# Optimization experiments

Hardware: AMD Instinct MI355X
Metric: run time of the kernel (lower is better)

## Reference

```python
import jax, jax.numpy as jnp
import numpy as np

H = 512        # hidden_dim
D_IN = 512     # input_dim
N_ACT = 16     # output_dim
DICT = 8192    # dict_len (episodic memory slots)
B = 4096       # batch
N_CYCLES = 10  # LCA iterations
DT_T = 0.6     # LCA dt/tau
EPS = 1e-8     # cosine-similarity eps


def setup_inputs() -> dict:
    key = jax.random.key(0)
    ks = jax.random.split(key, 12)
    NHT = 4 * H + 3  # (N_VSIG+1)*H + N_SSIG
    s = lambda i, shape, sc=1.0: jax.random.normal(ks[i], shape, jnp.float32) * sc
    return {
        "x_t": s(0, (1, B, D_IN)),
        "h_prev": s(1, (1, B, H), 0.1),
        "c_prev": s(2, (1, B, H), 0.1),
        "W_i2h": s(3, (NHT, D_IN), 1.0 / np.sqrt(D_IN)),
        "b_i2h": jnp.zeros((NHT,), jnp.float32),
        "W_h2h": s(4, (NHT, H), 1.0 / np.sqrt(H)),
        "b_h2h": jnp.zeros((NHT,), jnp.float32),
        "vals": s(5, (DICT, H), 0.1),  # episodic memory table
        "W_ih": s(6, (H, H), 1.0 / np.sqrt(H)),
        "b_ih": jnp.zeros((H,), jnp.float32),
        "W_actor": s(7, (N_ACT, H), 1.0 / np.sqrt(H)),
        "b_actor": jnp.zeros((N_ACT,), jnp.float32),
        "W_critic": s(8, (1, H), 1.0 / np.sqrt(H)),
        "b_critic": jnp.zeros((1,), jnp.float32),
        "mem_ptr": 0,
    }


def _lca(sim, leak, comp, w_input):
    # Leaky competing accumulator over memory slots; sim:[B,DICT], scalars:[B,1]
    ff = w_input * sim
    def step(V, _):
        inhib = comp * (jnp.sum(V, axis=-1, keepdims=True) - V)  # lateral inhibition (excl. self)
        V = jax.nn.relu(V + DT_T * (ff - leak * V - inhib))
        return V, None
    V, _ = jax.lax.scan(step, jnp.zeros_like(sim), None, length=N_CYCLES)
    return V


def reference(x_t, h_prev, c_prev, W_i2h, b_i2h, W_h2h, b_h2h, vals,
              W_ih, b_ih, W_actor, b_actor, W_critic, b_critic, mem_ptr):
    x, h, c = x_t[0], h_prev[0], c_prev[0]  # [B, dim]
    preact = x @ W_i2h.T + b_i2h + h @ W_h2h.T + b_h2h  # [B, 4H+3]
    gates = jax.nn.sigmoid(preact[:, :3 * H])
    f_t = gates[:, :H]
    o_t = gates[:, H:2 * H]
    i_t = gates[:, 2 * H:3 * H]
    inps = jax.nn.sigmoid(preact[:, 3 * H + 0])[:, None]  # input strength (gain=1)
    leak = jax.nn.sigmoid(preact[:, 3 * H + 1])[:, None]
    comp = jax.nn.sigmoid(preact[:, 3 * H + 2])[:, None]
    c_new = jnp.tanh(preact[:, 3 * H + 3:])
    c_t = c * f_t + i_t * c_new
    # --- recall: cosine similarity vs memory, then LCA competition ---
    qn = jnp.linalg.norm(c_t, axis=-1, keepdims=True)        # [B,1]
    mn = jnp.linalg.norm(vals, axis=-1, keepdims=True)       # [DICT,1]
    sim = (c_t @ vals.T) / jnp.maximum(qn * mn.T, EPS)       # [B,DICT]
    w = _lca(sim, leak, comp, inps)                          # [B,DICT]
    m_t = w @ vals                                           # [B,H]
    cm_t = c_t + m_t
    # --- encode: ring-buffer scatter write of cm_t into memory ---
    idx = (mem_ptr + jnp.arange(B)) % DICT
    new_vals = vals.at[idx].set(cm_t)
    h_t = o_t * jnp.tanh(cm_t)
    # --- A2C head ---
    a2c_h = jax.nn.relu(h_t @ W_ih.T + b_ih)
    pi = jax.nn.softmax(a2c_h @ W_actor.T + b_actor, axis=-1)
    value = a2c_h @ W_critic.T + b_critic
    return pi, value, h_t, cm_t, m_t, new_vals
```

## Files before the change

### kernel.cpp

```cpp
#include <hip/hip_runtime.h>
#include <hip/hip_fp16.h>
#include <math.h>

#define HH    512
#define DICT  8192
#define BATCH 4096
#define NCYC  10
#define DTT   0.6f

#define BM  128
#define BKT 64

using f16x8 = __attribute__((ext_vector_type(8))) _Float16;
using f32x4 = __attribute__((ext_vector_type(4))) float;

__device__ __forceinline__ float sigmoidf_(float x) { return 1.0f / (1.0f + __expf(-x)); }

__device__ __forceinline__ float waveReduceSum(float v) {
#pragma unroll
  for (int o = 1; o < 64; o <<= 1) v += __shfl_xor(v, o);
  return v;
}

__device__ __forceinline__ void gld16(const void* g, void* l) {
  __builtin_amdgcn_global_load_lds(
      (const __attribute__((address_space(1))) void*)g,
      (__attribute__((address_space(3))) void*)l, 16, 0, 0);
}

template<int N> __device__ __forceinline__ void vmwait() {
  if constexpr (N == 8)      asm volatile("s_waitcnt vmcnt(8)" ::: "memory");
  else if constexpr (N == 6) asm volatile("s_waitcnt vmcnt(6)" ::: "memory");
  else if constexpr (N == 4) asm volatile("s_waitcnt vmcnt(4)" ::: "memory");
  else if constexpr (N == 3) asm volatile("s_waitcnt vmcnt(3)" ::: "memory");
  else                       asm volatile("s_waitcnt vmcnt(0)" ::: "memory");
  __builtin_amdgcn_sched_barrier(0);
}

__device__ __forceinline__ void blockbar() {
  asm volatile("" ::: "memory");
  __builtin_amdgcn_s_barrier();
  __builtin_amdgcn_sched_barrier(0);
}

template<int ROWS>
__device__ __forceinline__ void stage_tile(const __half* gbase, int ld, char* lds, int tid) {
  constexpr int ISS = ROWS * 8 / 256;
#pragma unroll
  for (int i = 0; i < ISS; ++i) {
    int cidx = i * 256 + tid;
    int row  = cidx >> 3;
    int slot = cidx & 7;
    int k4   = slot ^ (row & 7);
    gld16(gbase + (size_t)row * ld + k4 * 8, lds + cidx * 16);
  }
}

__device__ __forceinline__ f16x8 frag_ld(const char* lds, int row, int kchunk) {
  int slot = kchunk ^ (row & 7);
  return *(const f16x8*)(lds + row * 128 + slot * 16);
}

template<int FN>
__device__ __forceinline__ void tile_mfma(const char* As, const char* Bs,
                                          int lane, int wr, int wc, f32x4 (&acc)[4][FN]) {
  const int g = lane >> 4, r = lane & 15;
#pragma unroll
  for (int ks = 0; ks < 2; ++ks) {
    f16x8 af[4], bfr[FN];
#pragma unroll
    for (int i = 0; i < 4; ++i)
      af[i] = frag_ld(As, wr * 64 + i * 16 + r, ks * 4 + g);
#pragma unroll
    for (int j = 0; j < FN; ++j)
      bfr[j] = frag_ld(Bs, wc * (FN * 16) + j * 16 + r, ks * 4 + g);
#pragma unroll
    for (int i = 0; i < 4; ++i)
#pragma unroll
      for (int j = 0; j < FN; ++j)
        acc[i][j] = __builtin_amdgcn_mfma_f32_16x16x32_f16(af[i], bfr[j], acc[i][j], 0, 0, 0);
  }
}

template<int BN, int FN>
__device__ __forceinline__ void gemm_seg(const __half* A, int lda, const __half* B, int ldb,
                                         int m0, int n0, int K, char* lds, int tid,
                                         f32x4 (&acc)[4][FN]) {
  constexpr int ABYTES = BM * BKT * 2;
  constexpr int BBYTES = BN * BKT * 2;
  constexpr int BUF = ABYTES + BBYTES;
  constexpr int NL = (BM + BN) * 8 / 256;
  const int lane = tid & 63, wid = tid >> 6;
  const int wr = wid >> 1, wc = wid & 1;
  const int nt = K / BKT;
  const __half* Ab = A + (size_t)m0 * lda;
  const __half* Bb = B + (size_t)n0 * ldb;
  stage_tile<BM>(Ab, lda, lds, tid);
  stage_tile<BN>(Bb, ldb, lds + ABYTES, tid);
  int cur = 0;
  for (int t = 0; t < nt; ++t) {
    char* curb = lds + cur * BUF;
    if (t + 1 < nt) {
      char* nxt = lds + (cur ^ 1) * BUF;
      stage_tile<BM>(Ab + (t + 1) * BKT, lda, nxt, tid);
      stage_tile<BN>(Bb + (t + 1) * BKT, ldb, nxt + ABYTES, tid);
      vmwait<NL>();
    } else {
      vmwait<0>();
    }
    blockbar();
    tile_mfma<FN>(curb, curb + ABYTES, lane, wr, wc, acc);
    blockbar();
    cur ^= 1;
  }
}

__device__ __forceinline__ void zero_acc4(f32x4 (&a)[4][4]) {
  f32x4 z = {0.f, 0.f, 0.f, 0.f};
#pragma unroll
  for (int i = 0; i < 4; ++i)
#pragma unroll
    for (int j = 0; j < 4; ++j) a[i][j] = z;
}
__device__ __forceinline__ void zero_acc2(f32x4 (&a)[4][2]) {
  f32x4 z = {0.f, 0.f, 0.f, 0.f};
#pragma unroll
  for (int i = 0; i < 4; ++i)
#pragma unroll
    for (int j = 0; j < 2; ++j) a[i][j] = z;
}

template<int ROWS, int NT>
__device__ __forceinline__ void stage32(const __half* gbase, int ld, char* lds, int tid) {
  constexpr int HALF = ROWS / 2;
  constexpr int ISS = ROWS * 4 / NT;
#pragma unroll
  for (int i = 0; i < ISS; ++i) {
    int cidx = i * NT + tid;
    int line = cidx >> 3;
    int slot = cidx & 7;
    int t    = slot ^ (line & 7);
    int row  = line + HALF * (t >> 2);
    int k4   = t & 3;
    gld16(gbase + (size_t)row * ld + k4 * 8, lds + cidx * 16);
  }
}

template<int HALF>
__device__ __forceinline__ f16x8 frag32(const char* lds, int row, int g) {
  int line = row & (HALF - 1);
  int t    = g + 4 * (row / HALF);
  int slot = t ^ (line & 7);
  return *(const f16x8*)(lds + line * 128 + slot * 16);
}

template<int MF, int NF, int AHALF, int BHALF>
__device__ __forceinline__ void tile_mfma32(const char* As, const char* Bs,
                                            int arow0, int brow0, int lane,
                                            f32x4 (&acc)[MF][NF]) {
  const int g = lane >> 4, r = lane & 15;
  f16x8 af[MF], bf[NF];
#pragma unroll
  for (int i = 0; i < MF; ++i) af[i] = frag32<AHALF>(As, arow0 + i * 16 + r, g);
#pragma unroll
  for (int j = 0; j < NF; ++j) bf[j] = frag32<BHALF>(Bs, brow0 + j * 16 + r, g);
#pragma unroll
  for (int i = 0; i < MF; ++i)
#pragma unroll
    for (int j = 0; j < NF; ++j)
      acc[i][j] = __builtin_amdgcn_mfma_f32_16x16x32_f16(af[i], bf[j], acc[i][j], 0, 0, 0);
}

__global__ __launch_bounds__(256) void k_prep(
    const float* __restrict__ x, const float* __restrict__ h,
    const float* __restrict__ Wi, const float* __restrict__ Wh, const float* __restrict__ Wih,
    const float* __restrict__ vals, const int* __restrict__ mptr,
    __half* __restrict__ x_h, __half* __restrict__ h_h,
    __half* __restrict__ Wip_h, __half* __restrict__ Whp_h, __half* __restrict__ Wih_h,
    float* __restrict__ nv, __half* __restrict__ vals_h, float* __restrict__ rmn,
    __half* __restrict__ vT) {
  __shared__ float tile[32][33];
  const int bid = blockIdx.x;
  if (bid < 6400) {
    int gq = bid * 256 + threadIdx.x;
    const float* src; __half* dst; int si, di;
    if (gq < 524288) {
      src = x; dst = x_h; si = di = gq * 4;
    } else if (gq < 1048576) {
      src = h; dst = h_h; si = di = (gq - 524288) * 4;
    } else if (gq < 1310720) {
      int iq = gq - 1048576;
      int jp = iq >> 7, k4 = (iq & 127) << 2;
      int U = jp >> 6, g = (jp >> 4) & 3, r = jp & 15;
      int u = U * 16 + r;
      int orig = g * 512 + u + (g == 3 ? 3 : 0);
      src = Wi; dst = Wip_h; si = orig * 512 + k4; di = jp * 512 + k4;
    } else if (gq < 1572864) {
      int iq = gq - 1310720;
      int jp = iq >> 7, k4 = (iq & 127) << 2;
      int U = jp >> 6, g = (jp >> 4) & 3, r = jp & 15;
      int u = U * 16 + r;
      int orig = g * 512 + u + (g == 3 ? 3 : 0);
      src = Wh; dst = Whp_h; si = orig * 512 + k4; di = jp * 512 + k4;
    } else if (gq < 1638400) {
      int iq = gq - 1572864;
      src = Wih; dst = Wih_h; si = di = iq * 4;
    } else return;
    float4 v = *(const float4*)(src + si);
    *(__half2*)(dst + di)     = __floats2half2_rn(v.x, v.y);
    *(__half2*)(dst + di + 2) = __floats2half2_rn(v.z, v.w);
  } else if (bid < 8448) {
    const int row  = (bid - 6400) * 4 + (threadIdx.x >> 6);
    const int lane = threadIdx.x & 63;
    const float* vr = vals + (size_t)row * HH + lane * 8;
    float4 a = *(const float4*)(vr);
    float4 b = *(const float4*)(vr + 4);
    if (((row + DICT - mptr[0]) & (DICT - 1)) >= BATCH) {
      float* nvp = nv + (size_t)row * HH + lane * 8;
      *(float4*)(nvp)     = a;
      *(float4*)(nvp + 4) = b;
    }
    __half* vh = vals_h + (size_t)row * HH + lane * 8;
    *(__half2*)(vh)     = __floats2half2_rn(a.x, a.y);
    *(__half2*)(vh + 2) = __floats2half2_rn(a.z, a.w);
    *(__half2*)(vh + 4) = __floats2half2_rn(b.x, b.y);
    *(__half2*)(vh + 6) = __floats2half2_rn(b.z, b.w);
    float ss = a.x * a.x + a.y * a.y + a.z * a.z + a.w * a.w
             + b.x * b.x + b.y * b.y + b.z * b.z + b.w * b.w;
    ss = waveReduceSum(ss);
    if (lane == 0) rmn[row] = 1.f / fmaxf(sqrtf(ss), 1e-12f);
  } else {
    const int idx = bid - 8448;
    const int r0 = (idx & 255) * 32, c0 = (idx >> 8) * 32;
    const int tr = threadIdx.x >> 5, tc = threadIdx.x & 31;
#pragma unroll
    for (int p = 0; p < 4; ++p)
      tile[tr + p * 8][tc] = vals[(size_t)(r0 + tr + p * 8) * HH + c0 + tc];
    __syncthreads();
#pragma unroll
    for (int p = 0; p < 4; ++p)
      vT[(size_t)(c0 + tr + p * 8) * DICT + r0 + tc] = __float2half(tile[tc][tr + p * 8]);
  }
}

__global__ __launch_bounds__(256) void k_preact(
    const __half* __restrict__ x_h, const __half* __restrict__ h_h,
    const __half* __restrict__ Wip, const __half* __restrict__ Whp,
    const float* __restrict__ bi, const float* __restrict__ bh,
    const float* __restrict__ c_prev,
    float* __restrict__ ct, float* __restrict__ ot, __half* __restrict__ ct_h) {
  __shared__ char smem[2 * (BM * BKT * 2 + 128 * BKT * 2)] __attribute__((aligned(16)));
  const int tid = threadIdx.x;
  const int m0 = blockIdx.y * 128, n0 = blockIdx.x * 128;
  f32x4 acc[4][4]; zero_acc4(acc);
  gemm_seg<128, 4>(x_h, HH, Wip, HH, m0, n0, HH, smem, tid, acc);
  gemm_seg<128, 4>(h_h, HH, Whp, HH, m0, n0, HH, smem, tid, acc);
  const int lane = tid & 63, wid = tid >> 6, wr = wid >> 1, wc = wid & 1;
  const int r = lane & 15;
  const int u = ((n0 >> 6) + wc) * 16 + r;
  float bsum[4];
#pragma unroll
  for (int g = 0; g < 4; ++g) {
    int orig = g * 512 + u + (g == 3 ? 3 : 0);
    bsum[g] = bi[orig] + bh[orig];
  }
#pragma unroll
  for (int fi = 0; fi < 4; ++fi)
#pragma unroll
    for (int q = 0; q < 4; ++q) {
      int m = m0 + wr * 64 + fi * 16 + (lane >> 4) * 4 + q;
      float f  = sigmoidf_(acc[fi][0][q] + bsum[0]);
      float o  = sigmoidf_(acc[fi][1][q] + bsum[1]);
      float ii = sigmoidf_(acc[fi][2][q] + bsum[2]);
      float cn = tanhf(acc[fi][3][q] + bsum[3]);
      size_t off = (size_t)m * HH + u;
      float cc = c_prev[off] * f + ii * cn;
      ct[off] = cc; ot[off] = o; ct_h[off] = __float2half(cc);
    }
}

__global__ __launch_bounds__(256) void k_scalars(
    const float* __restrict__ x, const float* __restrict__ h,
    const float* __restrict__ Wi, const float* __restrict__ Wh,
    const float* __restrict__ bi, const float* __restrict__ bh,
    const float* __restrict__ ct,
    float* __restrict__ inps, float* __restrict__ leak,
    float* __restrict__ comp, float* __restrict__ rqn) {
  const int b = blockIdx.x, wid = threadIdx.x >> 6, lane = threadIdx.x & 63;
  const int j = lane * 8;
  if (wid < 3) {
    const float* wi = Wi + (size_t)(1536 + wid) * HH + j;
    const float* wh = Wh + (size_t)(1536 + wid) * HH + j;
    const float* xr = x + (size_t)b * HH + j;
    const float* hr = h + (size_t)b * HH + j;
    float4 xa = *(const float4*)(xr), xb = *(const float4*)(xr + 4);
    float4 wa = *(const float4*)(wi), wb = *(const float4*)(wi + 4);
    float4 ha = *(const float4*)(hr), hb = *(const float4*)(hr + 4);
    float4 va = *(const float4*)(wh), vb = *(const float4*)(wh + 4);
    float s = xa.x * wa.x + xa.y * wa.y + xa.z * wa.z + xa.w * wa.w
            + xb.x * wb.x + xb.y * wb.y + xb.z * wb.z + xb.w * wb.w
            + ha.x * va.x + ha.y * va.y + ha.z * va.z + ha.w * va.w
            + hb.x * vb.x + hb.y * vb.y + hb.z * vb.z + hb.w * vb.w;
    s = waveReduceSum(s);
    if (lane == 0) {
      float v = sigmoidf_(s + bi[1536 + wid] + bh[1536 + wid]);
      if (wid == 0) inps[b] = v; else if (wid == 1) leak[b] = v; else comp[b] = v;
    }
  } else {
    const float* cr = ct + (size_t)b * HH + j;
    float4 a = *(const float4*)(cr), d = *(const float4*)(cr + 4);
    float ss = a.x * a.x + a.y * a.y + a.z * a.z + a.w * a.w
             + d.x * d.x + d.y * d.y + d.z * d.z + d.w * d.w;
    ss = waveReduceSum(ss);
    if (lane == 0) rqn[b] = 1.f / fmaxf(sqrtf(ss), 1e-12f);
  }
}

__global__ __launch_bounds__(512, 2) void k_sim(
    const __half* __restrict__ ct_h, const __half* __restrict__ vals_h,
    const float* __restrict__ rqn, const float* __restrict__ rmn,
    __half* __restrict__ sim_h) {
  __shared__ char smem[65536] __attribute__((aligned(16)));
  const int tid = threadIdx.x, lane = tid & 63, wid = tid >> 6;
  const int wr = wid >> 2, wc = wid & 3;
  const int bid = blockIdx.x;
  const int xcd = bid & 7, idx = bid >> 3;
  const int m0 = (xcd * 2 + (idx & 1)) * 256;
  const int n0 = (idx >> 1) * 256;
  f32x4 acc[8][4];
  { f32x4 z = {0.f, 0.f, 0.f, 0.f};
#pragma unroll
    for (int i = 0; i < 8; ++i)
#pragma unroll
      for (int j = 0; j < 4; ++j) acc[i][j] = z; }
  const __half* Ab = ct_h + (size_t)m0 * HH;
  const __half* Bb = vals_h + (size_t)n0 * HH;
  stage32<256, 512>(Ab, HH, smem, tid);
  stage32<256, 512>(Bb, HH, smem + 16384, tid);
  int cur = 0;
  for (int t = 0; t < 16; ++t) {
    char* curb = smem + cur * 32768;
    if (t < 15) {
      char* nxt = smem + (cur ^ 1) * 32768;
      stage32<256, 512>(Ab + (t + 1) * 32, HH, nxt, tid);
      stage32<256, 512>(Bb + (t + 1) * 32, HH, nxt + 16384, tid);
      vmwait<4>();
    } else {
      vmwait<0>();
    }
    blockbar();
    __builtin_amdgcn_s_setprio(1);
    tile_mfma32<8, 4, 128, 128>(curb, curb + 16384, wr * 128, wc * 64, lane, acc);
    __builtin_amdgcn_s_setprio(0);
    blockbar();
    cur ^= 1;
  }
  float* T = (float*)smem;
  const int g = lane >> 4, r = lane & 15;
  const int lrow = tid >> 4, seg = (tid & 15) * 16;
  float rmv[16];
  *(float4*)(rmv)      = *(const float4*)(rmn + n0 + seg);
  *(float4*)(rmv + 4)  = *(const float4*)(rmn + n0 + seg + 4);
  *(float4*)(rmv + 8)  = *(const float4*)(rmn + n0 + seg + 8);
  *(float4*)(rmv + 12) = *(const float4*)(rmn + n0 + seg + 12);
#pragma unroll
  for (int fi = 0; fi < 8; ++fi) {
    if (fi) __syncthreads();
#pragma unroll
    for (int fj = 0; fj < 4; ++fj)
#pragma unroll
      for (int q = 0; q < 4; ++q)
        T[(wr * 16 + g * 4 + q) * 260 + wc * 64 + fj * 16 + r] = acc[fi][fj][q];
    __syncthreads();
    int m = m0 + (lrow >> 4) * 128 + fi * 16 + (lrow & 15);
    float rq = rqn[m];
    const float* Tr = T + lrow * 260 + seg;
    f16x8 o0, o1;
#pragma unroll
    for (int j = 0; j < 8; ++j) o0[j] = (_Float16)(Tr[j] * rq * rmv[j]);
#pragma unroll
    for (int j = 0; j < 8; ++j) o1[j] = (_Float16)(Tr[8 + j] * rq * rmv[8 + j]);
    *(f16x8*)(sim_h + (size_t)m * DICT + n0 + seg)     = o0;
    *(f16x8*)(sim_h + (size_t)m * DICT + n0 + seg + 8) = o1;
  }
}

__global__ __launch_bounds__(256) void k_lca(
    const __half* __restrict__ sim_h, const float* __restrict__ inps,
    const float* __restrict__ leak, const float* __restrict__ comp,
    __half* __restrict__ w_h) {
  const int b = blockIdx.x, t = threadIdx.x;
  const __half* srow = sim_h + (size_t)b * DICT + t * 32;
  const float ffs = DTT * inps[b];
  const float a   = 1.0f - DTT * leak[b] + DTT * comp[b];
  const float cdt = DTT * comp[b];
  float ff[32], V[32];
#pragma unroll
  for (int i = 0; i < 4; ++i) {
    f16x8 v8 = *(const f16x8*)(srow + i * 8);
#pragma unroll
    for (int j = 0; j < 8; ++j) { ff[i * 8 + j] = ffs * (float)v8[j]; V[i * 8 + j] = 0.f; }
  }
  __shared__ float ps[4];
  for (int it = 0; it < NCYC; ++it) {
    float s = 0.f;
#pragma unroll
    for (int i = 0; i < 32; ++i) s += V[i];
    s = waveReduceSum(s);
    if ((t & 63) == 0) ps[t >> 6] = s;
    __syncthreads();
    float S = ps[0] + ps[1] + ps[2] + ps[3];
    __syncthreads();
    float sub = cdt * S;
#pragma unroll
    for (int i = 0; i < 32; ++i) V[i] = fmaxf(fmaf(a, V[i], ff[i] - sub), 0.f);
  }
  __half* wrow = w_h + (size_t)b * DICT + t * 32;
#pragma unroll
  for (int i = 0; i < 4; ++i) {
    f16x8 o8;
#pragma unroll
    for (int j = 0; j < 8; ++j) o8[j] = (_Float16)V[i * 8 + j];
    *(f16x8*)(wrow + i * 8) = o8;
  }
}

__global__ __launch_bounds__(512, 2) void k_mt_p(
    const __half* __restrict__ w_h, const __half* __restrict__ vT_h,
    float* __restrict__ partial) {
  __shared__ char smem[49152] __attribute__((aligned(16)));
  const int tid = threadIdx.x, lane = tid & 63, wid = tid >> 6;
  const int wr = wid >> 1, wc = wid & 1;
  const int bid = blockIdx.x;
  const int s = bid & 7, idx = bid >> 3;
  const int n = idx & 3, m = idx >> 2;
  const int m0 = m * 256, n0 = n * 128;
  f32x4 acc[4][4]; zero_acc4(acc);
  const __half* Ab = w_h + (size_t)m0 * DICT + s * 1024;
  const __half* Bb = vT_h + (size_t)n0 * DICT + s * 1024;
  stage32<256, 512>(Ab, DICT, smem, tid);
  stage32<128, 512>(Bb, DICT, smem + 16384, tid);
  int cur = 0;
  for (int t = 0; t < 32; ++t) {
    char* curb = smem + cur * 24576;
    if (t < 31) {
      char* nxt = smem + (cur ^ 1) * 24576;
      stage32<256, 512>(Ab + (t + 1) * 32, DICT, nxt, tid);
      stage32<128, 512>(Bb + (t + 1) * 32, DICT, nxt + 16384, tid);
      vmwait<3>();
    } else {
      vmwait<0>();
    }
    blockbar();
    __builtin_amdgcn_s_setprio(1);
    tile_mfma32<4, 4, 128, 64>(curb, curb + 16384, wr * 64, wc * 64, lane, acc);
    __builtin_amdgcn_s_setprio(0);
    blockbar();
    cur ^= 1;
  }
  float* T = (float*)smem;
  const int g = lane >> 4, r = lane & 15;
  const int lrow = tid >> 3, seg = (tid & 7) * 16;
  float* pbase = partial + (size_t)s * (BATCH * HH);
#pragma unroll
  for (int fi = 0; fi < 4; ++fi) {
    if (fi) __syncthreads();
#pragma unroll
    for (int fj = 0; fj < 4; ++fj)
#pragma unroll
      for (int q = 0; q < 4; ++q)
        T[(wr * 16 + g * 4 + q) * 132 + wc * 64 + fj * 16 + r] = acc[fi][fj][q];
    __syncthreads();
    int mm = m0 + (lrow >> 4) * 64 + fi * 16 + (lrow & 15);
    const float* Tr = T + lrow * 132 + seg;
    float* dst = pbase + (size_t)mm * HH + n0 + seg;
    *(float4*)(dst)      = *(const float4*)(Tr);
    *(float4*)(dst + 4)  = *(const float4*)(Tr + 4);
    *(float4*)(dst + 8)  = *(const float4*)(Tr + 8);
    *(float4*)(dst + 12) = *(const float4*)(Tr + 12);
  }
}

__global__ __launch_bounds__(256) void k_mt_red(
    const float* __restrict__ partial,
    const float* __restrict__ ct, const float* __restrict__ ot, const int* __restrict__ mptr,
    float* __restrict__ out_mt, float* __restrict__ out_cmt, float* __restrict__ out_ht,
    float* __restrict__ out_nv, __half* __restrict__ ht_h) {
  const int i4 = blockIdx.x * 256 + threadIdx.x;
  const size_t off = (size_t)i4 * 4;
  const int m = i4 >> 7;
  float4 p = *(const float4*)(partial + off);
#pragma unroll
  for (int s = 1; s < 8; ++s) {
    float4 q = *(const float4*)(partial + (size_t)s * 2097152 + off);
    p.x += q.x; p.y += q.y; p.z += q.z; p.w += q.w;
  }
  float4 c4 = *(const float4*)(ct + off);
  float4 o4 = *(const float4*)(ot + off);
  float4 cm, hv;
  cm.x = c4.x + p.x; hv.x = o4.x * tanhf(cm.x);
  cm.y = c4.y + p.y; hv.y = o4.y * tanhf(cm.y);
  cm.z = c4.z + p.z; hv.z = o4.z * tanhf(cm.z);
  cm.w = c4.w + p.w; hv.w = o4.w * tanhf(cm.w);
  *(float4*)(out_mt + off)  = p;
  *(float4*)(out_cmt + off) = cm;
  *(float4*)(out_ht + off)  = hv;
  *(__half2*)(ht_h + off)     = __floats2half2_rn(hv.x, hv.y);
  *(__half2*)(ht_h + off + 2) = __floats2half2_rn(hv.z, hv.w);
  const int nvrow = (mptr[0] + m) & (DICT - 1);
  *(float4*)(out_nv + (size_t)nvrow * HH + (off & 511)) = cm;
}

__global__ __launch_bounds__(256) void k_a2c(
    const __half* __restrict__ ht_h, const __half* __restrict__ Wih_h,
    const float* __restrict__ bih, float* __restrict__ a2c) {
  __shared__ char smem[2 * (BM * BKT * 2 + 64 * BKT * 2)] __attribute__((aligned(16)));
  const int tid = threadIdx.x;
  const int bid = blockIdx.x;
  const int xn = (bid >> 3) & 7, ym = (bid & 7) | ((bid >> 6) << 3);
  const int m0 = ym * 128, n0 = xn * 64;
  f32x4 acc[4][2]; zero_acc2(acc);
  gemm_seg<64, 2>(ht_h, HH, Wih_h, HH, m0, n0, HH, smem, tid, acc);
  const int lane = tid & 63, wid = tid >> 6, wr = wid >> 1, wc = wid & 1;
  float* T = (float*)smem;
  const int gg = lane >> 4, r = lane & 15;
  const int lrow = tid >> 3, c8 = (tid & 7) * 8;
  float4 b0 = *(const float4*)(bih + n0 + c8);
  float4 b1 = *(const float4*)(bih + n0 + c8 + 4);
#pragma unroll
  for (int fi = 0; fi < 4; ++fi) {
    if (fi) __syncthreads();
#pragma unroll
    for (int fj = 0; fj < 2; ++fj)
#pragma unroll
      for (int qq = 0; qq < 4; ++qq)
        T[(wr * 16 + gg * 4 + qq) * 68 + wc * 32 + fj * 16 + r] = acc[fi][fj][qq];
    __syncthreads();
    int mm = m0 + (lrow >> 4) * 64 + fi * 16 + (lrow & 15);
    float4 v0 = *(const float4*)(T + lrow * 68 + c8);
    float4 v1 = *(const float4*)(T + lrow * 68 + c8 + 4);
    v0.x = fmaxf(v0.x + b0.x, 0.f); v0.y = fmaxf(v0.y + b0.y, 0.f);
    v0.z = fmaxf(v0.z + b0.z, 0.f); v0.w = fmaxf(v0.w + b0.w, 0.f);
    v1.x = fmaxf(v1.x + b1.x, 0.f); v1.y = fmaxf(v1.y + b1.y, 0.f);
    v1.z = fmaxf(v1.z + b1.z, 0.f); v1.w = fmaxf(v1.w + b1.w, 0.f);
    float* dst = a2c + (size_t)mm * HH + n0 + c8;
    *(float4*)dst       = v0;
    *(float4*)(dst + 4) = v1;
  }
}

__global__ __launch_bounds__(256) void k_actor(
    const float* __restrict__ a2c,
    const float* __restrict__ Wact, const float* __restrict__ bact,
    const float* __restrict__ Wcr, const float* __restrict__ bcr,
    float* __restrict__ out_pi, float* __restrict__ out_val) {
  const int b = blockIdx.x * 4 + (threadIdx.x >> 6);
  const int lane = threadIdx.x & 63;
  const float* hrow = a2c + (size_t)b * HH;
  float4 a0 = *(const float4*)(hrow + (lane << 3));
  float4 a1 = *(const float4*)(hrow + (lane << 3) + 4);
  float lg[17];
#pragma unroll
  for (int o = 0; o < 17; ++o) {
    const float* wr = (o < 16) ? (Wact + (size_t)o * HH) : Wcr;
    float4 w0 = *(const float4*)(wr + (lane << 3));
    float4 w1 = *(const float4*)(wr + (lane << 3) + 4);
    float s = a0.x * w0.x + a0.y * w0.y + a0.z * w0.z + a0.w * w0.w
            + a1.x * w1.x + a1.y * w1.y + a1.z * w1.z + a1.w * w1.w;
    lg[o] = waveReduceSum(s);
  }
#pragma unroll
  for (int o = 0; o < 16; ++o) lg[o] += bact[o];
  float mx = lg[0];
#pragma unroll
  for (int o = 1; o < 16; ++o) mx = fmaxf(mx, lg[o]);
  float e[16], sum = 0.f;
#pragma unroll
  for (int o = 0; o < 16; ++o) { e[o] = __expf(lg[o] - mx); sum += e[o]; }
  float rs = 1.f / sum;
  if (lane == 0) {
#pragma unroll
    for (int o = 0; o < 16; ++o) out_pi[(size_t)b * 16 + o] = e[o] * rs;
    out_val[b] = lg[16] + bcr[0];
  }
}

extern "C" void kernel_launch(void* const* d_in, const int* in_sizes, int n_in,
                              void* d_out, int out_size, void* d_ws, size_t ws_size,
                              hipStream_t stream) {
  const float* x    = (const float*)d_in[0];
  const float* h    = (const float*)d_in[1];
  const float* c    = (const float*)d_in[2];
  const float* Wi   = (const float*)d_in[3];
  const float* bi   = (const float*)d_in[4];
  const float* Wh   = (const float*)d_in[5];
  const float* bh   = (const float*)d_in[6];
  const float* vals = (const float*)d_in[7];
  const float* Wih  = (const float*)d_in[8];
  const float* bih  = (const float*)d_in[9];
  const float* Wact = (const float*)d_in[10];
  const float* bact = (const float*)d_in[11];
  const float* Wcr  = (const float*)d_in[12];
  const float* bcr  = (const float*)d_in[13];
  const int*   mptr = (const int*)d_in[14];

  float* F = (float*)d_ws;
  __half* w_h    = (__half*)F;
  __half* sim_h   = (__half*)(F + 16777216);
  float*  a2c     = F + 16777216;
  float*  partial = F + 33554432;
  float*  ct     = F + 50331648;
  float*  ot     = F + 52428800;
  __half* ct_h   = (__half*)(F + 54525952);
  __half* vals_h = (__half*)(F + 55574528);
  __half* vT_h   = (__half*)(F + 57671680);
  __half* x_h    = (__half*)(F + 59768832);
  __half* ht_h   = x_h;
  __half* h_h    = (__half*)(F + 60817408);
  __half* Wip_h  = (__half*)(F + 61865984);
  __half* Whp_h  = (__half*)(F + 62423040);
  __half* Wih_h  = (__half*)(F + 62980096);
  float*  inps   = F + 63111168;
  float*  leak   = inps + 4096;
  float*  comp   = leak + 4096;
  float*  rqn    = comp + 4096;
  float*  rmn    = rqn + 4096;

  float* out     = (float*)d_out;
  float* out_pi  = out;
  float* out_val = out + 65536;
  float* out_ht  = out + 69632;
  float* out_cmt = out_ht + 2097152;
  float* out_mt  = out_cmt + 2097152;
  float* out_nv  = out_mt + 2097152;

  dim3 b256(256);
  dim3 b512(512);
  k_prep   <<<12544, b256, 0, stream>>>(x, h, Wi, Wh, Wih, vals, mptr,
                                        x_h, h_h, Wip_h, Whp_h, Wih_h,
                                        out_nv, vals_h, rmn, vT_h);
  k_preact <<<dim3(16, 32), b256, 0, stream>>>(x_h, h_h, Wip_h, Whp_h, bi, bh, c,
                                               ct, ot, ct_h);
  k_scalars<<<BATCH, b256, 0, stream>>>(x, h, Wi, Wh, bi, bh, ct, inps, leak, comp, rqn);
  k_sim    <<<512, b512, 0, stream>>>(ct_h, vals_h, rqn, rmn, sim_h);
  k_lca    <<<BATCH, b256, 0, stream>>>(sim_h, inps, leak, comp, w_h);
  k_mt_p   <<<512, b512, 0, stream>>>(w_h, vT_h, partial);
  k_mt_red <<<2048, b256, 0, stream>>>(partial, ct, ot, mptr,
                                       out_mt, out_cmt, out_ht, out_nv, ht_h);
  k_a2c    <<<256, b256, 0, stream>>>(ht_h, Wih_h, bih, a2c);
  k_actor  <<<BATCH / 4, b256, 0, stream>>>(a2c, Wact, bact, Wcr, bcr, out_pi, out_val);
}
```

Before: 241.1 us.

## Rewrite sim and m_t GEMMs with 8-phase half-tile pipelined LDS staging

Replaces the simple double-buffered 32-wide K staging in k_sim and k_mt_p with a shared gemm_8ph routine. It stages 64-wide K tiles in 128-row halves and interleaves each half-load with MFMA phases over a 128KB dynamic LDS double buffer. k_mt_p moves to 256x256 tiles (256 blocks) and k_sim changes its tile-to-XCD mapping so XCDs share B tiles. The intent is finer-grained overlap of global-to-LDS loads with MFMA and better operand reuse. The cost is heavier LDS use, which limits occupancy, and halving k_mt_p's grid may leave CUs underused.

```diff
diff --git a/kernel.cpp b/kernel.cpp
--- a/kernel.cpp
+++ b/kernel.cpp
@@ -31,8 +31,7 @@
 template<int N> __device__ __forceinline__ void vmwait() {
   if constexpr (N == 8)      asm volatile("s_waitcnt vmcnt(8)" ::: "memory");
   else if constexpr (N == 6) asm volatile("s_waitcnt vmcnt(6)" ::: "memory");
-  else if constexpr (N == 4) asm volatile("s_waitcnt vmcnt(4)" ::: "memory");
-  else if constexpr (N == 3) asm volatile("s_waitcnt vmcnt(3)" ::: "memory");
+  else if constexpr (N == 2) asm volatile("s_waitcnt vmcnt(2)" ::: "memory");
   else                       asm volatile("s_waitcnt vmcnt(0)" ::: "memory");
   __builtin_amdgcn_sched_barrier(0);
 }
@@ -130,45 +129,97 @@
     for (int j = 0; j < 2; ++j) a[i][j] = z;
 }
 
-template<int ROWS, int NT>
-__device__ __forceinline__ void stage32(const __half* gbase, int ld, char* lds, int tid) {
-  constexpr int HALF = ROWS / 2;
-  constexpr int ISS = ROWS * 4 / NT;
-#pragma unroll
-  for (int i = 0; i < ISS; ++i) {
-    int cidx = i * NT + tid;
-    int line = cidx >> 3;
+__device__ __forceinline__ void stage_half(const __half* tilebase, int ld, char* ldstile,
+                                           int h, int kcol, int tid) {
+#pragma unroll
+  for (int i = 0; i < 2; ++i) {
+    int cidx = i * 512 + tid;
+    int lrow = cidx >> 3;
     int slot = cidx & 7;
-    int t    = slot ^ (line & 7);
-    int row  = line + HALF * (t >> 2);
-    int k4   = t & 3;
-    gld16(gbase + (size_t)row * ld + k4 * 8, lds + cidx * 16);
-  }
-}
-
-template<int HALF>
-__device__ __forceinline__ f16x8 frag32(const char* lds, int row, int g) {
-  int line = row & (HALF - 1);
-  int t    = g + 4 * (row / HALF);
-  int slot = t ^ (line & 7);
-  return *(const f16x8*)(lds + line * 128 + slot * 16);
-}
-
-template<int MF, int NF, int AHALF, int BHALF>
-__device__ __forceinline__ void tile_mfma32(const char* As, const char* Bs,
-                                            int arow0, int brow0, int lane,
-                                            f32x4 (&acc)[MF][NF]) {
-  const int g = lane >> 4, r = lane & 15;
-  f16x8 af[MF], bf[NF];
-#pragma unroll
-  for (int i = 0; i < MF; ++i) af[i] = frag32<AHALF>(As, arow0 + i * 16 + r, g);
-#pragma unroll
-  for (int j = 0; j < NF; ++j) bf[j] = frag32<BHALF>(Bs, brow0 + j * 16 + r, g);
-#pragma unroll
-  for (int i = 0; i < MF; ++i)
-#pragma unroll
-    for (int j = 0; j < NF; ++j)
-      acc[i][j] = __builtin_amdgcn_mfma_f32_16x16x32_f16(af[i], bf[j], acc[i][j], 0, 0, 0);
+    int row  = h * 128 + lrow;
+    int k4   = slot ^ (row & 7);
+    gld16(tilebase + (size_t)row * ld + kcol + k4 * 8,
+          ldstile + row * 128 + slot * 16);
+  }
+}
+
+__device__ __forceinline__ f16x8 fragA8(const char* At, int fi, int wr, int ks, int lane) {
+  int r = lane & 15, g = lane >> 4;
+  int row = fi * 32 + wr * 16 + r;
+  int slot = (ks * 4 + g) ^ (row & 7);
+  return *(const f16x8*)(At + row * 128 + slot * 16);
+}
+__device__ __forceinline__ f16x8 fragB8(const char* Bt, int j, int wc, int ks, int lane) {
+  int r = lane & 15, g = lane >> 4;
+  int row = wc * 64 + j * 16 + r;
+  int slot = (ks * 4 + g) ^ (row & 7);
+  return *(const f16x8*)(Bt + row * 128 + slot * 16);
+}
+
+#define PHASE(TT, KS, MH, RB)                                                  \
+  {                                                                            \
+    if (RB) {                                                                  \
+      _Pragma("unroll")                                                        \
+      for (int j = 0; j < 4; ++j) bf[j] = fragB8((TT) + 32768, j, wc, KS, lane); \
+    }                                                                          \
+    f16x8 af[4];                                                               \
+    _Pragma("unroll")                                                          \
+    for (int i = 0; i < 4; ++i) af[i] = fragA8((TT), (MH)*4 + i, wr, KS, lane); \
+    __builtin_amdgcn_s_setprio(1);                                             \
+    _Pragma("unroll")                                                          \
+    for (int i = 0; i < 4; ++i)                                                \
+      _Pragma("unroll")                                                        \
+      for (int j = 0; j < 4; ++j)                                              \
+        acc[(MH)*4 + i][j] = __builtin_amdgcn_mfma_f32_16x16x32_f16(           \
+            af[i], bf[j], acc[(MH)*4 + i][j], 0, 0, 0);                        \
+    __builtin_amdgcn_s_setprio(0);                                             \
+  }
+
+template<int NT>
+__device__ __forceinline__ void gemm_8ph(const __half* At, int lda,
+                                         const __half* Bt, int ldb,
+                                         char* lds, int tid, f32x4 (&acc)[8][4]) {
+  const int lane = tid & 63, wid = tid >> 6;
+  const int wr = wid >> 2, wc = wid & 3;
+  char* b0 = lds;
+  char* b1 = lds + 65536;
+  stage_half(At, lda, b0, 0, 0, tid);
+  stage_half(At, lda, b0, 1, 0, tid);
+  stage_half(Bt, ldb, b0 + 32768, 0, 0, tid);
+  stage_half(Bt, ldb, b0 + 32768, 1, 0, tid);
+  stage_half(At, lda, b1, 0, 64, tid);
+  constexpr int ITERS = NT / 2;
+  f16x8 bf[4];
+#pragma unroll 1
+  for (int it = 0; it < ITERS; ++it) {
+    const int kt = 2 * it;
+    const bool stg = (it < ITERS - 1);
+    vmwait<2>(); blockbar();
+    stage_half(At, lda, b1, 1, (kt + 1) * 64, tid);
+    PHASE(b0, 0, 0, true)
+    blockbar();
+    stage_half(Bt, ldb, b1 + 32768, 0, (kt + 1) * 64, tid);
+    PHASE(b0, 0, 1, false)
+    blockbar();
+    stage_half(Bt, ldb, b1 + 32768, 1, (kt + 1) * 64, tid);
+    PHASE(b0, 1, 0, true)
+    blockbar();
+    if (stg) stage_half(At, lda, b0, 0, (kt + 2) * 64, tid);
+    PHASE(b0, 1, 1, false)
+    if (stg) { vmwait<2>(); } else { vmwait<0>(); }
+    blockbar();
+    if (stg) stage_half(At, lda, b0, 1, (kt + 2) * 64, tid);
+    PHASE(b1, 0, 0, true)
+    blockbar();
+    if (stg) stage_half(Bt, ldb, b0 + 32768, 0, (kt + 2) * 64, tid);
+    PHASE(b1, 0, 1, false)
+    blockbar();
+    if (stg) stage_half(Bt, ldb, b0 + 32768, 1, (kt + 2) * 64, tid);
+    PHASE(b1, 1, 0, true)
+    blockbar();
+    if (stg) stage_half(At, lda, b1, 0, (kt + 3) * 64, tid);
+    PHASE(b1, 1, 1, false)
+  }
 }
 
 __global__ __launch_bounds__(256) void k_prep(
@@ -320,42 +371,22 @@
     const __half* __restrict__ ct_h, const __half* __restrict__ vals_h,
     const float* __restrict__ rqn, const float* __restrict__ rmn,
     __half* __restrict__ sim_h) {
-  __shared__ char smem[65536] __attribute__((aligned(16)));
+  extern __shared__ char dsm[];
   const int tid = threadIdx.x, lane = tid & 63, wid = tid >> 6;
   const int wr = wid >> 2, wc = wid & 3;
   const int bid = blockIdx.x;
   const int xcd = bid & 7, idx = bid >> 3;
-  const int m0 = (xcd * 2 + (idx & 1)) * 256;
-  const int n0 = (idx >> 1) * 256;
+  const int nt_ = xcd * 4 + (idx & 3);
+  const int mt_ = idx >> 2;
+  const int m0 = mt_ * 256, n0 = nt_ * 256;
   f32x4 acc[8][4];
   { f32x4 z = {0.f, 0.f, 0.f, 0.f};
 #pragma unroll
     for (int i = 0; i < 8; ++i)
 #pragma unroll
       for (int j = 0; j < 4; ++j) acc[i][j] = z; }
-  const __half* Ab = ct_h + (size_t)m0 * HH;
-  const __half* Bb = vals_h + (size_t)n0 * HH;
-  stage32<256, 512>(Ab, HH, smem, tid);
-  stage32<256, 512>(Bb, HH, smem + 16384, tid);
-  int cur = 0;
-  for (int t = 0; t < 16; ++t) {
-    char* curb = smem + cur * 32768;
-    if (t < 15) {
-      char* nxt = smem + (cur ^ 1) * 32768;
-      stage32<256, 512>(Ab + (t + 1) * 32, HH, nxt, tid);
-      stage32<256, 512>(Bb + (t + 1) * 32, HH, nxt + 16384, tid);
-      vmwait<4>();
-    } else {
-      vmwait<0>();
-    }
-    blockbar();
-    __builtin_amdgcn_s_setprio(1);
-    tile_mfma32<8, 4, 128, 128>(curb, curb + 16384, wr * 128, wc * 64, lane, acc);
-    __builtin_amdgcn_s_setprio(0);
-    blockbar();
-    cur ^= 1;
-  }
-  float* T = (float*)smem;
+  gemm_8ph<8>(ct_h + (size_t)m0 * HH, HH, vals_h + (size_t)n0 * HH, HH, dsm, tid, acc);
+  float* T = (float*)dsm;
   const int g = lane >> 4, r = lane & 15;
   const int lrow = tid >> 4, seg = (tid & 15) * 16;
   float rmv[16];
@@ -363,16 +394,17 @@
   *(float4*)(rmv + 4)  = *(const float4*)(rmn + n0 + seg + 4);
   *(float4*)(rmv + 8)  = *(const float4*)(rmn + n0 + seg + 8);
   *(float4*)(rmv + 12) = *(const float4*)(rmn + n0 + seg + 12);
-#pragma unroll
+  __syncthreads();
+#pragma unroll 1
   for (int fi = 0; fi < 8; ++fi) {
     if (fi) __syncthreads();
 #pragma unroll
-    for (int fj = 0; fj < 4; ++fj)
+    for (int j = 0; j < 4; ++j)
 #pragma unroll
       for (int q = 0; q < 4; ++q)
-        T[(wr * 16 + g * 4 + q) * 260 + wc * 64 + fj * 16 + r] = acc[fi][fj][q];
+        T[(wr * 16 + g * 4 + q) * 260 + wc * 64 + j * 16 + r] = acc[fi][j][q];
     __syncthreads();
-    int m = m0 + (lrow >> 4) * 128 + fi * 16 + (lrow & 15);
+    int m = m0 + fi * 32 + lrow;
     float rq = rqn[m];
     const float* Tr = T + lrow * 260 + seg;
     f16x8 o0, o1;
@@ -428,51 +460,37 @@
 __global__ __launch_bounds__(512, 2) void k_mt_p(
     const __half* __restrict__ w_h, const __half* __restrict__ vT_h,
     float* __restrict__ partial) {
-  __shared__ char smem[49152] __attribute__((aligned(16)));
+  extern __shared__ char dsm[];
   const int tid = threadIdx.x, lane = tid & 63, wid = tid >> 6;
-  const int wr = wid >> 1, wc = wid & 1;
+  const int wr = wid >> 2, wc = wid & 3;
   const int bid = blockIdx.x;
   const int s = bid & 7, idx = bid >> 3;
-  const int n = idx & 3, m = idx >> 2;
-  const int m0 = m * 256, n0 = n * 128;
-  f32x4 acc[4][4]; zero_acc4(acc);
-  const __half* Ab = w_h + (size_t)m0 * DICT + s * 1024;
-  const __half* Bb = vT_h + (size_t)n0 * DICT + s * 1024;
-  stage32<256, 512>(Ab, DICT, smem, tid);
-  stage32<128, 512>(Bb, DICT, smem + 16384, tid);
-  int cur = 0;
-  for (int t = 0; t < 32; ++t) {
-    char* curb = smem + cur * 24576;
-    if (t < 31) {
-      char* nxt = smem + (cur ^ 1) * 24576;
-      stage32<256, 512>(Ab + (t + 1) * 32, DICT, nxt, tid);
-      stage32<128, 512>(Bb + (t + 1) * 32, DICT, nxt + 16384, tid);
-      vmwait<3>();
-    } else {
-      vmwait<0>();
-    }
-    blockbar();
-    __builtin_amdgcn_s_setprio(1);
-    tile_mfma32<4, 4, 128, 64>(curb, curb + 16384, wr * 64, wc * 64, lane, acc);
-    __builtin_amdgcn_s_setprio(0);
-    blockbar();
-    cur ^= 1;
-  }
-  float* T = (float*)smem;
+  const int n = idx & 1, m = idx >> 1;
+  const int m0 = m * 256, n0 = n * 256;
+  f32x4 acc[8][4];
+  { f32x4 z = {0.f, 0.f, 0.f, 0.f};
+#pragma unroll
+    for (int i = 0; i < 8; ++i)
+#pragma unroll
+      for (int j = 0; j < 4; ++j) acc[i][j] = z; }
+  gemm_8ph<16>(w_h + (size_t)m0 * DICT + s * 1024, DICT,
+               vT_h + (size_t)n0 * DICT + s * 1024, DICT, dsm, tid, acc);
+  float* T = (float*)dsm;
   const int g = lane >> 4, r = lane & 15;
-  const int lrow = tid >> 3, seg = (tid & 7) * 16;
+  const int lrow = tid >> 4, seg = (tid & 15) * 16;
   float* pbase = partial + (size_t)s * (BATCH * HH);
-#pragma unroll
-  for (int fi = 0; fi < 4; ++fi) {
+  __syncthreads();
+#pragma unroll 1
+  for (int fi = 0; fi < 8; ++fi) {
     if (fi) __syncthreads();
 #pragma unroll
-    for (int fj = 0; fj < 4; ++fj)
+    for (int j = 0; j < 4; ++j)
 #pragma unroll
       for (int q = 0; q < 4; ++q)
-        T[(wr * 16 + g * 4 + q) * 132 + wc * 64 + fj * 16 + r] = acc[fi][fj][q];
+        T[(wr * 16 + g * 4 + q) * 260 + wc * 64 + j * 16 + r] = acc[fi][j][q];
     __syncthreads();
-    int mm = m0 + (lrow >> 4) * 64 + fi * 16 + (lrow & 15);
-    const float* Tr = T + lrow * 132 + seg;
+    int mm = m0 + fi * 32 + lrow;
+    const float* Tr = T + lrow * 260 + seg;
     float* dst = pbase + (size_t)mm * HH + n0 + seg;
     *(float4*)(dst)      = *(const float4*)(Tr);
     *(float4*)(dst + 4)  = *(const float4*)(Tr + 4);
@@ -634,6 +652,11 @@
   float* out_mt  = out_cmt + 2097152;
   float* out_nv  = out_mt + 2097152;
 
+  (void)hipFuncSetAttribute(reinterpret_cast<const void*>(k_sim),
+                            hipFuncAttributeMaxDynamicSharedMemorySize, 131072);
+  (void)hipFuncSetAttribute(reinterpret_cast<const void*>(k_mt_p),
+                            hipFuncAttributeMaxDynamicSharedMemorySize, 131072);
+
   dim3 b256(256);
   dim3 b512(512);
   k_prep   <<<12544, b256, 0, stream>>>(x, h, Wi, Wh, Wih, vals, mptr,
@@ -642,9 +665,9 @@
   k_preact <<<dim3(16, 32), b256, 0, stream>>>(x_h, h_h, Wip_h, Whp_h, bi, bh, c,
                                                ct, ot, ct_h);
   k_scalars<<<BATCH, b256, 0, stream>>>(x, h, Wi, Wh, bi, bh, ct, inps, leak, comp, rqn);
-  k_sim    <<<512, b512, 0, stream>>>(ct_h, vals_h, rqn, rmn, sim_h);
+  k_sim    <<<512, b512, 131072, stream>>>(ct_h, vals_h, rqn, rmn, sim_h);
   k_lca    <<<BATCH, b256, 0, stream>>>(sim_h, inps, leak, comp, w_h);
-  k_mt_p   <<<512, b512, 0, stream>>>(w_h, vT_h, partial);
+  k_mt_p   <<<256, b512, 131072, stream>>>(w_h, vT_h, partial);
   k_mt_red <<<2048, b256, 0, stream>>>(partial, ct, ot, mptr,
                                        out_mt, out_cmt, out_ht, out_nv, ht_h);
   k_a2c    <<<256, b256, 0, stream>>>(ht_h, Wih_h, bih, a2c);
```

Measured after the change: 323.6 us. +34.2%, slower.
